# Kernel optimization log

Measured on AMD Instinct MI355X. Metric: run time of the kernel, lower is better.

Reference implementation:

```python
import jax, jax.numpy as jnp
import numpy as np
from jax import lax

DIM = 256
NUM_HEADS = 8
SW = 7
HEAD_DIM = DIM // NUM_HEADS
SCALE = HEAD_DIM ** -0.5


def setup_inputs() -> dict:
    key = jax.random.key(0)
    ks = jax.random.split(key, 7)
    B, C, H, W = 8, DIM, 56, 56
    x = jax.random.normal(ks[0], (B, C, H, W), dtype=jnp.float32)
    w_qkv = jax.random.normal(ks[1], (3 * C, C), dtype=jnp.float32) * 0.02
    b_qkv = jnp.zeros((3 * C,), dtype=jnp.float32)
    # depthwise 3x3 kernel, OIHW with feature_group_count=C -> (C,1,3,3)
    w_dw = jax.random.normal(ks[2], (C, 1, 3, 3), dtype=jnp.float32) * 0.02
    b_dw = jnp.zeros((C,), dtype=jnp.float32)
    w_proj = jax.random.normal(ks[3], (C, C), dtype=jnp.float32) * 0.02
    b_proj = jnp.zeros((C,), dtype=jnp.float32)
    return {"x": x, "w_qkv": w_qkv, "b_qkv": b_qkv, "w_dw": w_dw,
            "b_dw": b_dw, "w_proj": w_proj, "b_proj": b_proj}


def _conv1x1(x, w, b):
    # x:[B,C,H,W], w:[O,C] -> [B,O,H,W]
    return jnp.einsum('bchw,oc->bohw', x, w) + b[None, :, None, None]


def _dwconv3x3(x, w, b):
    C = x.shape[1]
    y = lax.conv_general_dilated(x, w, window_strides=(1, 1), padding='SAME',
                                 dimension_numbers=('NCHW', 'OIHW', 'NCHW'),
                                 feature_group_count=C)
    return y + b[None, :, None, None]


def _stripe_attn_H(q, k, v, sw):
    # q,k,v: [B,h,C,H,W]; local attention within sw-thick horizontal stripes
    B, h, C, H, W = q.shape
    sw = min(sw, H)
    pad = (-H) % sw
    if pad:
        pw = [(0, 0)] * 3 + [(0, pad), (0, 0)]
        q = jnp.pad(q, pw); k = jnp.pad(k, pw); v = jnp.pad(v, pw)
    Hp = H + pad
    n = Hp // sw

    def rs(t):
        # -> [B,h,n, sw*W, C]
        return t.reshape(B, h, C, n, sw, W).transpose(0, 1, 3, 4, 5, 2).reshape(B, h, n, sw * W, C)

    qs, ks_, vs = rs(q) * SCALE, rs(k), rs(v)
    attn = jax.nn.softmax(jnp.einsum('bhnqc,bhnkc->bhnqk', qs, ks_), axis=-1)
    out = jnp.einsum('bhnqk,bhnkc->bhnqc', attn, vs)
    out = out.reshape(B, h, n, sw, W, C).transpose(0, 1, 5, 2, 3, 4).reshape(B, h, C, Hp, W)
    return out[:, :, :, :H, :]


def _stripe_attn_W(q, k, v, sw):
    # attention within sw-thick vertical stripes; softmax is permutation-
    # equivariant over the stripe sequence, so transposing H<->W and reusing
    # the H-stripe kernel computes identical math.
    t = lambda a: a.transpose(0, 1, 2, 4, 3)
    return t(_stripe_attn_H(t(q), t(k), t(v), sw))


def reference(x, w_qkv, b_qkv, w_dw, b_dw, w_proj, b_proj):
    B, C, H, W = x.shape
    hh = NUM_HEADS // 2
    qkv = _conv1x1(x, w_qkv, b_qkv)
    q, k, v = jnp.split(qkv, 3, axis=1)
    v = v + _dwconv3x3(v, w_dw, b_dw)

    def heads(t):
        return t.reshape(B, NUM_HEADS, HEAD_DIM, H, W)

    q, k, v = heads(q), heads(k), heads(v)
    out_h = _stripe_attn_H(q[:, :hh], k[:, :hh], v[:, :hh], SW)
    out_w = _stripe_attn_W(q[:, hh:], k[:, hh:], v[:, hh:], SW)
    out = jnp.concatenate([out_h, out_w], axis=1).reshape(B, C, H, W)
    return _conv1x1(out, w_proj, b_proj)
```

## Files before the change

### kernel.cpp

```cpp
#include <hip/hip_runtime.h>
#include <hip/hip_bf16.h>
#include <stdint.h>

#define Bn 8
#define Cn 256
#define Hn 56
#define Wn 56
#define HWn 3136
#define NHEADS 8
#define HDIM 32
#define SEQ 392
#define NSTR 8
#define QKV_LD 768
#define KSC (0.17677669529663689f * 1.4426950408889634f)

#if __has_builtin(__builtin_amdgcn_exp2f)
#define EXP2(x) __builtin_amdgcn_exp2f(x)
#else
#define EXP2(x) exp2f(x)
#endif

typedef short short8 __attribute__((ext_vector_type(8)));
typedef float floatx4 __attribute__((ext_vector_type(4)));

__device__ __forceinline__ unsigned short f2bf(float f) {
  union { float f; uint32_t u; } v; v.f = f;
  uint32_t u = v.u;
  u += 0x7fffu + ((u >> 16) & 1u);
  return (unsigned short)(u >> 16);
}
__device__ __forceinline__ float bf2f(unsigned short h) {
  union { uint32_t u; float f; } v; v.u = ((uint32_t)h) << 16;
  return v.f;
}
__device__ __forceinline__ uint32_t cvt_pk_bf16(float lo, float hi) {
  uint32_t r;
  asm("v_cvt_pk_bf16_f32 %0, %1, %2" : "=v"(r) : "v"(lo), "v"(hi));
  return r;
}
__device__ __forceinline__ void gload16(const unsigned short* g, unsigned short* l) {
  __builtin_amdgcn_global_load_lds((const __attribute__((address_space(1))) void*)g,
                                   (__attribute__((address_space(3))) void*)l, 16, 0, 0);
}

__global__ __launch_bounds__(256) void k_prep(const float* __restrict__ wa,
                                              const float* __restrict__ wb,
                                              unsigned short* __restrict__ da,
                                              unsigned short* __restrict__ db,
                                              const float* __restrict__ x,
                                              unsigned short* __restrict__ xt) {
  int bx = blockIdx.x;
  int t = threadIdx.x;
  if (bx < 256) {
    int i = bx * 256 + t;
    if (i < 49152) {
      float4 v = ((const float4*)wa)[i];
      ushort4 o;
      o.x = f2bf(v.x); o.y = f2bf(v.y); o.z = f2bf(v.z); o.w = f2bf(v.w);
      ((ushort4*)da)[i] = o;
    } else {
      int k = i - 49152;
      float4 v = ((const float4*)wb)[k];
      ushort4 o;
      o.x = f2bf(v.x); o.y = f2bf(v.y); o.z = f2bf(v.z); o.w = f2bf(v.w);
      ((ushort4*)db)[k] = o;
    }
    return;
  }
  __shared__ float tile[32][33];
  int tx = bx - 256;
  int pb = tx % 98, cb = (tx / 98) & 7, b = tx / 784;
  int c = t >> 3, p4 = (t & 7) * 4;
  float4 v = *(const float4*)(x + (((size_t)b * Cn + cb * 32 + c) * HWn + pb * 32 + p4));
  tile[c][p4 + 0] = v.x; tile[c][p4 + 1] = v.y; tile[c][p4 + 2] = v.z; tile[c][p4 + 3] = v.w;
  __syncthreads();
  int p = t >> 3, c4 = (t & 7) * 4;
  ushort4 o;
  o.x = f2bf(tile[c4 + 0][p]); o.y = f2bf(tile[c4 + 1][p]);
  o.z = f2bf(tile[c4 + 2][p]); o.w = f2bf(tile[c4 + 3][p]);
  *(ushort4*)(xt + (((size_t)b * HWn + pb * 32 + p) * Cn + cb * 32 + c4)) = o;
}

template <int EPI>
__global__ __launch_bounds__(512) void k_gemm(const unsigned short* __restrict__ A,
                                              const unsigned short* __restrict__ Bt,
                                              const float* __restrict__ bias,
                                              unsigned short* __restrict__ outB,
                                              float* __restrict__ outF,
                                              unsigned short* __restrict__ outV,
                                              int M, int N, int nm, int nper) {
  const int K = 256;
  __shared__ __align__(16) char SH[EPI ? 67584 : 65536];
  unsigned short* As = (unsigned short*)SH;
  unsigned short* Bs = As + 16384;
  int t = threadIdx.x;
  int raw = blockIdx.x;
  int chunk = gridDim.x >> 3;
  int wg = (raw & 7) * chunk + (raw >> 3);
  int b = wg / nper, r = wg % nper;
  int m0 = (r % nm) * 128, n0 = (r / nm) * 128;
  const unsigned short* Bb = Bt + (size_t)b * N * K;
  int lane = t & 63, w = t >> 6;
  int wr = w >> 1, wc = w & 1;
  int g = lane >> 4, q = lane & 15;
  int srow8 = lane >> 3;
  int slot = lane & 7;

  const unsigned short* Ag[2];
  const unsigned short* Bg[2];
  int ldst[2];
#pragma unroll
  for (int i = 0; i < 2; i++) {
    int row = i * 64 + w * 8 + srow8;
    int cs = slot ^ srow8;
    Ag[i] = A + (size_t)(m0 + row) * K + cs * 8;
    int nr = n0 + row;
    Bg[i] = Bb + (size_t)((nr < N) ? nr : (N - 1)) * K + cs * 8;
    ldst[i] = (i * 64 + w * 8) * 64;
  }

  floatx4 z4 = {0.f, 0.f, 0.f, 0.f};
  floatx4 acc[2][4];
#pragma unroll
  for (int i = 0; i < 2; i++)
#pragma unroll
    for (int j = 0; j < 4; j++) acc[i][j] = z4;

#define STAGE(kt, off) do {                                                    \
    _Pragma("unroll")                                                          \
    for (int i = 0; i < 2; i++) gload16(Ag[i] + (kt) * 64, &As[(off) + ldst[i]]); \
    _Pragma("unroll")                                                          \
    for (int i = 0; i < 2; i++) gload16(Bg[i] + (kt) * 64, &Bs[(off) + ldst[i]]); \
  } while (0)

#define COMPUTE(off) do {                                                      \
    _Pragma("unroll")                                                          \
    for (int kk = 0; kk < 64; kk += 32) {                                      \
      short8 af[2], bfr[4];                                                    \
      _Pragma("unroll")                                                        \
      for (int i = 0; i < 2; i++) {                                            \
        int row = wr * 32 + i * 16 + q;                                        \
        af[i] = *(const short8*)&As[(off) + row * 64 + ((((kk >> 3) + g) ^ (q & 7)) << 3)]; \
      }                                                                        \
      _Pragma("unroll")                                                        \
      for (int j = 0; j < 4; j++) {                                            \
        int row = wc * 64 + j * 16 + q;                                        \
        bfr[j] = *(const short8*)&Bs[(off) + row * 64 + ((((kk >> 3) + g) ^ (q & 7)) << 3)]; \
      }                                                                        \
      _Pragma("unroll")                                                        \
      for (int i = 0; i < 2; i++)                                              \
        _Pragma("unroll")                                                      \
        for (int j = 0; j < 4; j++)                                            \
          acc[i][j] = __builtin_amdgcn_mfma_f32_16x16x32_bf16(af[i], bfr[j], acc[i][j], 0, 0, 0); \
    }                                                                          \
  } while (0)

  STAGE(0, 0);
  STAGE(1, 8192);
  asm volatile("s_waitcnt vmcnt(4)" ::: "memory");
  __syncthreads();
  COMPUTE(0);
  __syncthreads();
  STAGE(2, 0);
  asm volatile("s_waitcnt vmcnt(4)" ::: "memory");
  __syncthreads();
  COMPUTE(8192);
  __syncthreads();
  STAGE(3, 8192);
  asm volatile("s_waitcnt vmcnt(4)" ::: "memory");
  __syncthreads();
  COMPUTE(0);
  asm volatile("s_waitcnt vmcnt(0)" ::: "memory");
  __syncthreads();
  COMPUTE(8192);
#undef STAGE
#undef COMPUTE

  __syncthreads();
  if (EPI == 0) {
    unsigned short* E = (unsigned short*)SH;
#pragma unroll
    for (int i = 0; i < 2; i++) {
      int ob = m0 + wr * 32 + i * 16 + g * 4;
      float bs0 = bias[ob + 0], bs1 = bias[ob + 1], bs2 = bias[ob + 2], bs3 = bias[ob + 3];
      float sc = (ob >= 256 && ob < 512) ? KSC : 1.0f;
      int lobg = wr * 4 + i * 2 + (g >> 1);
#pragma unroll
      for (int j = 0; j < 4; j++) {
        int lc = wc * 64 + j * 16 + q;
        ushort4 o;
        o.x = f2bf((acc[i][j][0] + bs0) * sc);
        o.y = f2bf((acc[i][j][1] + bs1) * sc);
        o.z = f2bf((acc[i][j][2] + bs2) * sc);
        o.w = f2bf((acc[i][j][3] + bs3) * sc);
        *(ushort4*)&E[lc * 128 + ((lobg ^ (lc & 7)) << 3) + (g & 1) * 4] = o;
      }
    }
    __syncthreads();
    int c = t >> 2, part = t & 3;
    int col = n0 + c;
    if (col < N) {
      int mt = m0 >> 7;
      unsigned short* dst;
      if (mt < 4) {
        int hd = (mt & 1) * 4 + part;
        int sl = (mt >> 1) * 8 + hd;
        int p_ord = (hd >= 4) ? ((col % Wn) * Wn + col / Wn) : col;
        dst = outB + (((size_t)b * 16 + sl) * HWn + p_ord) * 32;
      } else {
        dst = outV + ((size_t)b * HWn + col) * 256 + (m0 - 512) + part * 32;
      }
#pragma unroll
      for (int k2 = part * 4; k2 < part * 4 + 4; k2++) {
        short8 v = *(const short8*)&E[c * 128 + ((k2 ^ (c & 7)) << 3)];
        *(short8*)(dst + (k2 - part * 4) * 8) = v;
      }
    }
  } else {
    float* Ef = (float*)SH;
#pragma unroll
    for (int i = 0; i < 2; i++) {
      int ob = m0 + wr * 32 + i * 16 + g * 4;
      int lob = wr * 32 + i * 16 + g * 4;
      float bs0 = bias[ob + 0], bs1 = bias[ob + 1], bs2 = bias[ob + 2], bs3 = bias[ob + 3];
#pragma unroll
      for (int j = 0; j < 4; j++) {
        int lc = wc * 64 + j * 16 + q;
        Ef[(lob + 0) * 132 + lc] = acc[i][j][0] + bs0;
        Ef[(lob + 1) * 132 + lc] = acc[i][j][1] + bs1;
        Ef[(lob + 2) * 132 + lc] = acc[i][j][2] + bs2;
        Ef[(lob + 3) * 132 + lc] = acc[i][j][3] + bs3;
      }
    }
    __syncthreads();
    int rr = t >> 2, seg = t & 3;
    float* dst = outF + (size_t)b * M * N + (size_t)(m0 + rr) * N + n0;
#pragma unroll
    for (int k2 = 0; k2 < 8; k2++) {
      int col = seg * 32 + k2 * 4;
      if (n0 + col < N) {
        floatx4 v = *(const floatx4*)&Ef[rr * 132 + col];
        *(floatx4*)(dst + col) = v;
      }
    }
  }
}

__global__ __launch_bounds__(256) void k_dwconv_t(const unsigned short* __restrict__ vb,
                                                  const float* __restrict__ wdw,
                                                  const float* __restrict__ bdw,
                                                  unsigned short* __restrict__ vmt) {
  __shared__ float wS[1152];
  __shared__ float bS[128];
  __shared__ __align__(16) unsigned short tile[16][140];
  int t = threadIdx.x;
  int pass = blockIdx.y, b = blockIdx.z;
  for (int i = t; i < 1152; i += 256) wS[i] = wdw[pass * 1152 + i];
  if (t < 128) bS[t] = bdw[pass * 128 + t];
  __syncthreads();

  int pi = t >> 4, c8 = (t & 15) * 8;
  int i16 = blockIdx.x * 16 + pi;
  int h, w;
  if (pass == 0) { h = i16 / Wn; w = i16 % Wn; }
  else           { w = i16 / Hn; h = i16 % Hn; }

  const unsigned short* vq = vb + pass * 128 + c8;
  float a[8];
  short8 vc = *(const short8*)(vq + ((size_t)b * HWn + h * Wn + w) * 256);
#pragma unroll
  for (int e = 0; e < 8; e++) a[e] = bf2f((unsigned short)vc[e]) + bS[c8 + e];
#pragma unroll
  for (int ky = 0; ky < 3; ky++) {
    int hh = h + ky - 1;
    if (hh < 0 || hh >= Hn) continue;
#pragma unroll
    for (int kx = 0; kx < 3; kx++) {
      int ww = w + kx - 1;
      if (ww < 0 || ww >= Wn) continue;
      short8 vn = *(const short8*)(vq + ((size_t)b * HWn + hh * Wn + ww) * 256);
#pragma unroll
      for (int e = 0; e < 8; e++) a[e] += bf2f((unsigned short)vn[e]) * wS[(c8 + e) * 9 + ky * 3 + kx];
    }
  }
  short8 o;
#pragma unroll
  for (int e = 0; e < 8; e++) o[e] = (short)f2bf(a[e]);
  *(short8*)&tile[pi][c8] = o;
  __syncthreads();

  int dd = t >> 1, half = t & 1;
  short8 ov;
#pragma unroll
  for (int k2 = 0; k2 < 8; k2++) ov[k2] = (short)tile[half * 8 + k2][dd];
  *(short8*)(vmt + ((size_t)(b * Cn + pass * 128 + dd)) * HWn + blockIdx.x * 16 + half * 8) = ov;
}

__global__ __launch_bounds__(512) void k_attn(const unsigned short* __restrict__ qkh,
                                              const unsigned short* __restrict__ vmt,
                                              unsigned short* __restrict__ aout) {
  __shared__ __align__(16) unsigned short Ks[12288];
  __shared__ __align__(16) unsigned short Vf[12800];
  __shared__ __align__(16) unsigned short Pf[4096];
  int s = blockIdx.x;
  int hd = blockIdx.y & 7, b = blockIdx.y >> 3;
  int t = threadIdx.x, lane = t & 63, wv = t >> 6;
  bool wst = (hd >= 4);
  int q = lane & 15, g = lane >> 4;
  int sbase = s * SEQ;

  const unsigned short* qh = qkh + (((size_t)b * 16 + hd) * HWn + sbase) * 32;
  const unsigned short* kh = qkh + (((size_t)b * 16 + 8 + hd) * HWn + sbase) * 32;

  short8 qpre[4];
#pragma unroll
  for (int it = 0; it < 4; it++) {
    int qb = it * 8 + wv;
    int qi = qb * 16 + q;
    int qil = (qi < SEQ) ? qi : 391;
    qpre[it] = *(const short8*)(qh + (size_t)qil * 32 + g * 8);
  }

#pragma unroll
  for (int P = 0; P < 3; P++) {
    int key = P * 128 + (t >> 2);
    int gg = t & 3;
    short8 kv = *(const short8*)(kh + (size_t)key * 32 + gg * 8);
    *(short8*)&Ks[((((key >> 4) * 4 + gg) * 16) + (key & 15)) * 8] = kv;
  }
  short8 kf24;
  {
    int key = 384 + q; if (key > 391) key = 391;
    kf24 = *(const short8*)(kh + (size_t)key * 32 + g * 8);
  }
  const unsigned short* vg = vmt + ((size_t)(b * Cn + hd * HDIM)) * HWn + sbase;
  for (int idx = t; idx < 1600; idx += 512) {
    int d = idx / 50, Gc = idx % 50;
    short8 vv = *(const short8*)(vg + (size_t)d * HWn + Gc * 8);
    *(short8*)&Vf[(Gc * 32 + (d ^ (Gc & 7))) * 8] = vv;
  }
  __syncthreads();

  floatx4 z4 = {0.f, 0.f, 0.f, 0.f};
  unsigned short* Pw = &Pf[wv * 512];
  int gh = g >> 1, ge = (g & 1) * 4;

#pragma unroll
  for (int it = 0; it < 4; it++) {
    int qb = it * 8 + wv;
    if (qb >= 25) continue;
    int qi = qb * 16 + q;
    int qil = (qi < SEQ) ? qi : 391;
    short8 qf = qpre[it];

    floatx4 sacc[25];
    __builtin_amdgcn_s_setprio(1);
#pragma unroll
    for (int j = 0; j < 24; j++) {
      short8 kf = *(const short8*)&Ks[((j * 4 + g) * 16 + q) * 8];
      sacc[j] = __builtin_amdgcn_mfma_f32_16x16x32_bf16(kf, qf, z4, 0, 0, 0);
    }
    sacc[24] = __builtin_amdgcn_mfma_f32_16x16x32_bf16(kf24, qf, z4, 0, 0, 0);
    __builtin_amdgcn_s_setprio(0);
    if (g >= 2) { sacc[24][0] = sacc[24][1] = sacc[24][2] = sacc[24][3] = -3.0e38f; }

    float sm = 0.f;
#pragma unroll
    for (int j = 0; j < 25; j++) {
      float e0 = EXP2(sacc[j][0]); float e1 = EXP2(sacc[j][1]);
      float e2 = EXP2(sacc[j][2]); float e3 = EXP2(sacc[j][3]);
      sacc[j][0] = e0; sacc[j][1] = e1; sacc[j][2] = e2; sacc[j][3] = e3;
      sm += (e0 + e1) + (e2 + e3);
    }
    sm += __shfl_xor(sm, 16);
    sm += __shfl_xor(sm, 32);
    float rcp = 1.0f / sm;

#define WRITEP(cc) do {                                                        \
    enum { jbW = (2*(cc)+1 < 25) ? (2*(cc)+1) : 24 };                          \
    uint2 wA, wB;                                                              \
    wA.x = cvt_pk_bf16(sacc[2*(cc)][0], sacc[2*(cc)][1]);                      \
    wA.y = cvt_pk_bf16(sacc[2*(cc)][2], sacc[2*(cc)][3]);                      \
    if (2*(cc)+1 < 25) {                                                       \
      wB.x = cvt_pk_bf16(sacc[jbW][0], sacc[jbW][1]);                          \
      wB.y = cvt_pk_bf16(sacc[jbW][2], sacc[jbW][3]);                          \
    } else { wB.x = 0u; wB.y = 0u; }                                           \
    *(uint2*)&Pw[(gh * 16 + q) * 8 + ge] = wA;                                 \
    *(uint2*)&Pw[((2 + gh) * 16 + q) * 8 + ge] = wB;                           \
  } while (0)

    floatx4 o0 = z4, o1 = z4;
    WRITEP(0);
#pragma unroll
    for (int ch = 0; ch < 13; ch++) {
      asm volatile("s_waitcnt lgkmcnt(0)" ::: "memory");
      short8 pfr = *(const short8*)&Pw[(g * 16 + q) * 8];
      int Gc = ch * 4 + g; if (Gc > 49) Gc = 49;
      int sw = Gc & 7;
      short8 vf0 = *(const short8*)&Vf[(Gc * 32 + (q ^ sw)) * 8];
      short8 vf1 = *(const short8*)&Vf[(Gc * 32 + 16 + (q ^ sw)) * 8];
      if (ch < 12) {
        switch (ch + 1) {
          case 1: WRITEP(1); break;  case 2: WRITEP(2); break;
          case 3: WRITEP(3); break;  case 4: WRITEP(4); break;
          case 5: WRITEP(5); break;  case 6: WRITEP(6); break;
          case 7: WRITEP(7); break;  case 8: WRITEP(8); break;
          case 9: WRITEP(9); break;  case 10: WRITEP(10); break;
          case 11: WRITEP(11); break; case 12: WRITEP(12); break;
        }
      }
      __builtin_amdgcn_s_setprio(1);
      o0 = __builtin_amdgcn_mfma_f32_16x16x32_bf16(vf0, pfr, o0, 0, 0, 0);
      o1 = __builtin_amdgcn_mfma_f32_16x16x32_bf16(vf1, pfr, o1, 0, 0, 0);
      __builtin_amdgcn_s_setprio(0);
    }
#undef WRITEP

    if (qi < SEQ) {
      int pq = wst ? ((qil % Wn) * Wn + s * 7 + qil / Wn) : (sbase + qil);
      size_t ob = ((size_t)b * HWn + pq) * Cn + hd * HDIM;
      ushort4 u0, u1;
      u0.x = f2bf(o0[0] * rcp); u0.y = f2bf(o0[1] * rcp);
      u0.z = f2bf(o0[2] * rcp); u0.w = f2bf(o0[3] * rcp);
      u1.x = f2bf(o1[0] * rcp); u1.y = f2bf(o1[1] * rcp);
      u1.z = f2bf(o1[2] * rcp); u1.w = f2bf(o1[3] * rcp);
      *(ushort4*)(aout + ob + g * 4) = u0;
      *(ushort4*)(aout + ob + 16 + g * 4) = u1;
    }
  }
}

extern "C" void kernel_launch(void* const* d_in, const int* in_sizes, int n_in,
                              void* d_out, int out_size, void* d_ws, size_t ws_size,
                              hipStream_t stream) {
  const float* x     = (const float*)d_in[0];
  const float* wqkv  = (const float*)d_in[1];
  const float* bqkv  = (const float*)d_in[2];
  const float* wdw   = (const float*)d_in[3];
  const float* bdw   = (const float*)d_in[4];
  const float* wproj = (const float*)d_in[5];
  const float* bproj = (const float*)d_in[6];
  float* out = (float*)d_out;

  unsigned short* xt   = (unsigned short*)d_ws;
  unsigned short* wqb  = xt + (size_t)Bn * HWn * Cn;
  unsigned short* wpb  = wqb + 768 * 256;
  unsigned short* qkh  = wpb + 256 * 256;
  unsigned short* vb   = qkh + (size_t)Bn * 16 * HWn * 32;
  unsigned short* vmt  = vb + (size_t)Bn * HWn * Cn;
  unsigned short* aout = vmt + (size_t)Bn * HWn * Cn;

  k_prep<<<dim3(256 + 98 * 8 * Bn), 256, 0, stream>>>(wqkv, wproj, wqb, wpb, x, xt);
  k_gemm<0><<<dim3(1200), 512, 0, stream>>>(wqb, xt, bqkv, qkh, nullptr, vb, 768, HWn, 6, 150);
  k_dwconv_t<<<dim3(196, 2, Bn), 256, 0, stream>>>(vb, wdw, bdw, vmt);
  k_attn<<<dim3(NSTR, Bn * NHEADS), 512, 0, stream>>>(qkh, vmt, aout);
  k_gemm<1><<<dim3(400), 512, 0, stream>>>(wpb, aout, bproj, nullptr, out, nullptr, 256, HWn, 2, 50);
}
```

Baseline: 105.6 us.

## Specialize QKV GEMM with small-LDS double-buffered K pipeline; widen dwconv blocks

```diff
diff --git a/kernel.cpp b/kernel.cpp
--- a/kernel.cpp
+++ b/kernel.cpp
@@ -81,16 +81,124 @@
   *(ushort4*)(xt + (((size_t)b * HWn + pb * 32 + p) * Cn + cb * 32 + c4)) = o;
 }
 
-template <int EPI>
-__global__ __launch_bounds__(512) void k_gemm(const unsigned short* __restrict__ A,
-                                              const unsigned short* __restrict__ Bt,
-                                              const float* __restrict__ bias,
-                                              unsigned short* __restrict__ outB,
-                                              float* __restrict__ outF,
-                                              unsigned short* __restrict__ outV,
-                                              int M, int N, int nm, int nper) {
+__global__ __launch_bounds__(512) void k_gemm0(const unsigned short* __restrict__ A,
+                                               const unsigned short* __restrict__ Bt,
+                                               const float* __restrict__ bias,
+                                               unsigned short* __restrict__ qkh,
+                                               unsigned short* __restrict__ outV) {
+  const int K = 256, N = HWn;
+  __shared__ __align__(16) unsigned short SH[16384];
+  unsigned short* As = SH;
+  unsigned short* Bs = SH + 8192;
+  int t = threadIdx.x;
+  int raw = blockIdx.x;
+  int chunk = gridDim.x >> 3;
+  int wg = (raw & 7) * chunk + (raw >> 3);
+  int b = wg / 150, r = wg % 150;
+  int m0 = (r % 6) * 128, n0 = (r / 6) * 128;
+  const unsigned short* Bb = Bt + (size_t)b * N * K;
+  int lane = t & 63, w = t >> 6;
+  int wr = w >> 1, wc = w & 1;
+  int g = lane >> 4, q = lane & 15;
+  int rt = t >> 2, st = t & 3;
+  int cs = st ^ (rt & 3);
+  const unsigned short* Ag = A + (size_t)(m0 + rt) * K + cs * 8;
+  int nr = n0 + rt;
+  const unsigned short* Bg = Bb + (size_t)((nr < N) ? nr : (N - 1)) * K + cs * 8;
+  int ldst = t * 8;
+
+  floatx4 z4 = {0.f, 0.f, 0.f, 0.f};
+  floatx4 acc[2][4];
+#pragma unroll
+  for (int i = 0; i < 2; i++)
+#pragma unroll
+    for (int j = 0; j < 4; j++) acc[i][j] = z4;
+
+#define STAGE0(kt, off) do {                                                   \
+    gload16(Ag + (kt) * 32, &As[(off) + ldst]);                                \
+    gload16(Bg + (kt) * 32, &Bs[(off) + ldst]);                                \
+  } while (0)
+
+#define COMPUTE0(off) do {                                                     \
+    short8 af[2], bfr[4];                                                      \
+    _Pragma("unroll")                                                          \
+    for (int i = 0; i < 2; i++) {                                              \
+      int row = wr * 32 + i * 16 + q;                                          \
+      af[i] = *(const short8*)&As[(off) + row * 32 + ((g ^ (q & 3)) << 3)];    \
+    }                                                                          \
+    _Pragma("unroll")                                                          \
+    for (int j = 0; j < 4; j++) {                                              \
+      int row = wc * 64 + j * 16 + q;                                          \
+      bfr[j] = *(const short8*)&Bs[(off) + row * 32 + ((g ^ (q & 3)) << 3)];   \
+    }                                                                          \
+    _Pragma("unroll")                                                          \
+    for (int i = 0; i < 2; i++)                                                \
+      _Pragma("unroll")                                                        \
+      for (int j = 0; j < 4; j++)                                              \
+        acc[i][j] = __builtin_amdgcn_mfma_f32_16x16x32_bf16(af[i], bfr[j], acc[i][j], 0, 0, 0); \
+  } while (0)
+
+  STAGE0(0, 0);
+  STAGE0(1, 4096);
+#pragma unroll
+  for (int tt = 0; tt < 8; tt++) {
+    if (tt < 7) { asm volatile("s_waitcnt vmcnt(2)" ::: "memory"); }
+    else       { asm volatile("s_waitcnt vmcnt(0)" ::: "memory"); }
+    __syncthreads();
+    COMPUTE0((tt & 1) * 4096);
+    __syncthreads();
+    if (tt < 6) STAGE0(tt + 2, (tt & 1) * 4096);
+  }
+#undef STAGE0
+#undef COMPUTE0
+
+  unsigned short* E = SH;
+#pragma unroll
+  for (int i = 0; i < 2; i++) {
+    int ob = m0 + wr * 32 + i * 16 + g * 4;
+    float bs0 = bias[ob + 0], bs1 = bias[ob + 1], bs2 = bias[ob + 2], bs3 = bias[ob + 3];
+    float sc = (ob >= 256 && ob < 512) ? KSC : 1.0f;
+    int lobg = wr * 4 + i * 2 + (g >> 1);
+#pragma unroll
+    for (int j = 0; j < 4; j++) {
+      int lc = wc * 64 + j * 16 + q;
+      ushort4 o;
+      o.x = f2bf((acc[i][j][0] + bs0) * sc);
+      o.y = f2bf((acc[i][j][1] + bs1) * sc);
+      o.z = f2bf((acc[i][j][2] + bs2) * sc);
+      o.w = f2bf((acc[i][j][3] + bs3) * sc);
+      *(ushort4*)&E[lc * 128 + ((lobg ^ (lc & 7)) << 3) + (g & 1) * 4] = o;
+    }
+  }
+  __syncthreads();
+  int c = t >> 2, part = t & 3;
+  int col = n0 + c;
+  if (col < N) {
+    int mt = m0 >> 7;
+    unsigned short* dst;
+    if (mt < 4) {
+      int hd = (mt & 1) * 4 + part;
+      int sl = (mt >> 1) * 8 + hd;
+      int p_ord = (hd >= 4) ? ((col % Wn) * Wn + col / Wn) : col;
+      dst = qkh + (((size_t)b * 16 + sl) * HWn + p_ord) * 32;
+    } else {
+      dst = outV + ((size_t)b * HWn + col) * 256 + (m0 - 512) + part * 32;
+    }
+#pragma unroll
+    for (int k2 = part * 4; k2 < part * 4 + 4; k2++) {
+      short8 v = *(const short8*)&E[c * 128 + ((k2 ^ (c & 7)) << 3)];
+      *(short8*)(dst + (k2 - part * 4) * 8) = v;
+    }
+  }
+}
+
+__global__ __launch_bounds__(512) void k_gemm1(const unsigned short* __restrict__ A,
+                                               const unsigned short* __restrict__ Bt,
+                                               const float* __restrict__ bias,
+                                               float* __restrict__ outF,
+                                               int M, int N, int nm, int nper) {
   const int K = 256;
-  __shared__ __align__(16) char SH[EPI ? 67584 : 65536];
+  __shared__ __align__(16) char SH[67584];
   unsigned short* As = (unsigned short*)SH;
   unsigned short* Bs = As + 16384;
   int t = threadIdx.x;
@@ -177,93 +285,52 @@
 #undef COMPUTE
 
   __syncthreads();
-  if (EPI == 0) {
-    unsigned short* E = (unsigned short*)SH;
-#pragma unroll
-    for (int i = 0; i < 2; i++) {
-      int ob = m0 + wr * 32 + i * 16 + g * 4;
-      float bs0 = bias[ob + 0], bs1 = bias[ob + 1], bs2 = bias[ob + 2], bs3 = bias[ob + 3];
-      float sc = (ob >= 256 && ob < 512) ? KSC : 1.0f;
-      int lobg = wr * 4 + i * 2 + (g >> 1);
-#pragma unroll
-      for (int j = 0; j < 4; j++) {
-        int lc = wc * 64 + j * 16 + q;
-        ushort4 o;
-        o.x = f2bf((acc[i][j][0] + bs0) * sc);
-        o.y = f2bf((acc[i][j][1] + bs1) * sc);
-        o.z = f2bf((acc[i][j][2] + bs2) * sc);
-        o.w = f2bf((acc[i][j][3] + bs3) * sc);
-        *(ushort4*)&E[lc * 128 + ((lobg ^ (lc & 7)) << 3) + (g & 1) * 4] = o;
-      }
-    }
-    __syncthreads();
-    int c = t >> 2, part = t & 3;
-    int col = n0 + c;
-    if (col < N) {
-      int mt = m0 >> 7;
-      unsigned short* dst;
-      if (mt < 4) {
-        int hd = (mt & 1) * 4 + part;
-        int sl = (mt >> 1) * 8 + hd;
-        int p_ord = (hd >= 4) ? ((col % Wn) * Wn + col / Wn) : col;
-        dst = outB + (((size_t)b * 16 + sl) * HWn + p_ord) * 32;
-      } else {
-        dst = outV + ((size_t)b * HWn + col) * 256 + (m0 - 512) + part * 32;
-      }
-#pragma unroll
-      for (int k2 = part * 4; k2 < part * 4 + 4; k2++) {
-        short8 v = *(const short8*)&E[c * 128 + ((k2 ^ (c & 7)) << 3)];
-        *(short8*)(dst + (k2 - part * 4) * 8) = v;
-      }
-    }
-  } else {
-    float* Ef = (float*)SH;
-#pragma unroll
-    for (int i = 0; i < 2; i++) {
-      int ob = m0 + wr * 32 + i * 16 + g * 4;
-      int lob = wr * 32 + i * 16 + g * 4;
-      float bs0 = bias[ob + 0], bs1 = bias[ob + 1], bs2 = bias[ob + 2], bs3 = bias[ob + 3];
-#pragma unroll
-      for (int j = 0; j < 4; j++) {
-        int lc = wc * 64 + j * 16 + q;
-        Ef[(lob + 0) * 132 + lc] = acc[i][j][0] + bs0;
-        Ef[(lob + 1) * 132 + lc] = acc[i][j][1] + bs1;
-        Ef[(lob + 2) * 132 + lc] = acc[i][j][2] + bs2;
-        Ef[(lob + 3) * 132 + lc] = acc[i][j][3] + bs3;
-      }
-    }
-    __syncthreads();
-    int rr = t >> 2, seg = t & 3;
-    float* dst = outF + (size_t)b * M * N + (size_t)(m0 + rr) * N + n0;
-#pragma unroll
-    for (int k2 = 0; k2 < 8; k2++) {
-      int col = seg * 32 + k2 * 4;
-      if (n0 + col < N) {
-        floatx4 v = *(const floatx4*)&Ef[rr * 132 + col];
-        *(floatx4*)(dst + col) = v;
-      }
-    }
-  }
-}
-
-__global__ __launch_bounds__(256) void k_dwconv_t(const unsigned short* __restrict__ vb,
+  float* Ef = (float*)SH;
+#pragma unroll
+  for (int i = 0; i < 2; i++) {
+    int ob = m0 + wr * 32 + i * 16 + g * 4;
+    int lob = wr * 32 + i * 16 + g * 4;
+    float bs0 = bias[ob + 0], bs1 = bias[ob + 1], bs2 = bias[ob + 2], bs3 = bias[ob + 3];
+#pragma unroll
+    for (int j = 0; j < 4; j++) {
+      int lc = wc * 64 + j * 16 + q;
+      Ef[(lob + 0) * 132 + lc] = acc[i][j][0] + bs0;
+      Ef[(lob + 1) * 132 + lc] = acc[i][j][1] + bs1;
+      Ef[(lob + 2) * 132 + lc] = acc[i][j][2] + bs2;
+      Ef[(lob + 3) * 132 + lc] = acc[i][j][3] + bs3;
+    }
+  }
+  __syncthreads();
+  int rr = t >> 2, seg = t & 3;
+  float* dst = outF + (size_t)b * M * N + (size_t)(m0 + rr) * N + n0;
+#pragma unroll
+  for (int k2 = 0; k2 < 8; k2++) {
+    int col = seg * 32 + k2 * 4;
+    if (n0 + col < N) {
+      floatx4 v = *(const floatx4*)&Ef[rr * 132 + col];
+      *(floatx4*)(dst + col) = v;
+    }
+  }
+}
+
+__global__ __launch_bounds__(512) void k_dwconv_t(const unsigned short* __restrict__ vb,
                                                   const float* __restrict__ wdw,
                                                   const float* __restrict__ bdw,
                                                   unsigned short* __restrict__ vmt) {
   __shared__ float wS[1152];
   __shared__ float bS[128];
-  __shared__ __align__(16) unsigned short tile[16][140];
+  __shared__ __align__(16) unsigned short tile[32][140];
   int t = threadIdx.x;
   int pass = blockIdx.y, b = blockIdx.z;
-  for (int i = t; i < 1152; i += 256) wS[i] = wdw[pass * 1152 + i];
+  for (int i = t; i < 1152; i += 512) wS[i] = wdw[pass * 1152 + i];
   if (t < 128) bS[t] = bdw[pass * 128 + t];
   __syncthreads();
 
   int pi = t >> 4, c8 = (t & 15) * 8;
-  int i16 = blockIdx.x * 16 + pi;
+  int i32 = blockIdx.x * 32 + pi;
   int h, w;
-  if (pass == 0) { h = i16 / Wn; w = i16 % Wn; }
-  else           { w = i16 / Hn; h = i16 % Hn; }
+  if (pass == 0) { h = i32 / Wn; w = i32 % Wn; }
+  else           { w = i32 / Hn; h = i32 % Hn; }
 
   const unsigned short* vq = vb + pass * 128 + c8;
   float a[8];
@@ -289,11 +356,11 @@
   *(short8*)&tile[pi][c8] = o;
   __syncthreads();
 
-  int dd = t >> 1, half = t & 1;
+  int dd = t >> 2, quarter = t & 3;
   short8 ov;
 #pragma unroll
-  for (int k2 = 0; k2 < 8; k2++) ov[k2] = (short)tile[half * 8 + k2][dd];
-  *(short8*)(vmt + ((size_t)(b * Cn + pass * 128 + dd)) * HWn + blockIdx.x * 16 + half * 8) = ov;
+  for (int k2 = 0; k2 < 8; k2++) ov[k2] = (short)tile[quarter * 8 + k2][dd];
+  *(short8*)(vmt + ((size_t)(b * Cn + pass * 128 + dd)) * HWn + blockIdx.x * 32 + quarter * 8) = ov;
 }
 
 __global__ __launch_bounds__(512) void k_attn(const unsigned short* __restrict__ qkh,
@@ -451,8 +518,8 @@
   unsigned short* aout = vmt + (size_t)Bn * HWn * Cn;
 
   k_prep<<<dim3(256 + 98 * 8 * Bn), 256, 0, stream>>>(wqkv, wproj, wqb, wpb, x, xt);
-  k_gemm<0><<<dim3(1200), 512, 0, stream>>>(wqb, xt, bqkv, qkh, nullptr, vb, 768, HWn, 6, 150);
-  k_dwconv_t<<<dim3(196, 2, Bn), 256, 0, stream>>>(vb, wdw, bdw, vmt);
+  k_gemm0<<<dim3(1200), 512, 0, stream>>>(wqb, xt, bqkv, qkh, vb);
+  k_dwconv_t<<<dim3(98, 2, Bn), 512, 0, stream>>>(vb, wdw, bdw, vmt);
   k_attn<<<dim3(NSTR, Bn * NHEADS), 512, 0, stream>>>(qkh, vmt, aout);
-  k_gemm<1><<<dim3(400), 512, 0, stream>>>(wpb, aout, bproj, nullptr, out, nullptr, 256, HWn, 2, 50);
-}
+  k_gemm1<<<dim3(400), 512, 0, stream>>>(wpb, aout, bproj, out, 256, HWn, 2, 50);
+}
```

Result: no change. 105.0 us (-0.5%).
